# Kernel optimization log

Measured on AMD Instinct MI355X. Metric: run time of the kernel, lower is better.

Reference implementation:

```python
import jax, jax.numpy as jnp
import numpy as np

EMBED_DIM = 1024
NUM_HEADS = 16
HEAD_DIM = EMBED_DIM // NUM_HEADS
SCALE = HEAD_DIM ** -0.5


def setup_inputs() -> dict:
    key = jax.random.key(0)
    ks = jax.random.split(key, 5)
    B, N, C = 4, 2048, EMBED_DIM
    s = C ** -0.5
    return {
        "x": jax.random.normal(ks[0], (B, N, C), dtype=jnp.float32),
        "w_qkv": jax.random.normal(ks[1], (C, 3 * C), dtype=jnp.float32) * s,
        "b_qkv": jnp.zeros((3 * C,), dtype=jnp.float32),
        "w_proj": jax.random.normal(ks[2], (C, C), dtype=jnp.float32) * s,
        "b_proj": jnp.zeros((C,), dtype=jnp.float32),
    }


def reference(x, w_qkv, b_qkv, w_proj, b_proj):
    B, N, C = x.shape
    H, D = NUM_HEADS, HEAD_DIM
    qkv = x @ w_qkv + b_qkv                      # (B, N, 3C)
    qkv = qkv.reshape(B, N, 3, H, D)
    qkv = jnp.transpose(qkv, (2, 0, 3, 1, 4))    # (3, B, H, N, D)
    q, k, v = qkv[0], qkv[1], qkv[2]
    attn = jnp.einsum('bhnd,bhmd->bhnm', q, k) * SCALE
    attn = jax.nn.softmax(attn, axis=-1)
    out = jnp.einsum('bhnm,bhmd->bhnd', attn, v)  # (B, H, N, D)
    out = jnp.transpose(out, (0, 2, 1, 3)).reshape(B, N, C)
    return out @ w_proj + b_proj
```

## Files before the change

### kernel.cpp

```cpp
#include <hip/hip_runtime.h>

typedef __attribute__((ext_vector_type(8))) short short8v;
typedef __attribute__((ext_vector_type(4))) short short4v;
typedef __attribute__((ext_vector_type(4))) float float4v;
typedef __attribute__((ext_vector_type(4))) unsigned short ushort4v;
typedef __attribute__((ext_vector_type(8))) unsigned short ushort8v;

#define GLOBAL_AS __attribute__((address_space(1)))
#define LDS_AS __attribute__((address_space(3)))

__device__ __forceinline__ void async_cp16(const void* g, void* l) {
  __builtin_amdgcn_global_load_lds((const GLOBAL_AS void*)g, (LDS_AS void*)l, 16, 0, 0);
}

__device__ __forceinline__ unsigned short f2bf(float f) {
  unsigned u = __float_as_uint(f);
  u += 0x7fffu + ((u >> 16) & 1u);
  return (unsigned short)(u >> 16);
}

#if defined(__HIP_DEVICE_COMPILE__)
#if __has_builtin(__builtin_amdgcn_exp2f)
#define EXP2F(x) __builtin_amdgcn_exp2f(x)
#else
#define EXP2F(x) exp2f(x)
#endif
#else
#define EXP2F(x) exp2f(x)
#endif

#if defined(__HIP_DEVICE_COMPILE__) && __has_builtin(__builtin_amdgcn_cvt_pk_bf16_f32)
typedef __attribute__((ext_vector_type(2))) __bf16 bf16x2v;
__device__ __forceinline__ unsigned pk_bf16(float a, float b) {
  bf16x2v r = __builtin_amdgcn_cvt_pk_bf16_f32(a, b);
  return __builtin_bit_cast(unsigned, r);
}
#else
__device__ __forceinline__ unsigned pk_bf16(float a, float b) {
  return (unsigned)f2bf(a) | ((unsigned)f2bf(b) << 16);
}
#endif

#define MFMA_QK(a, b, c) __builtin_amdgcn_mfma_f32_16x16x32_bf16(a, b, c, 0, 0, 0)


__global__ __launch_bounds__(256) void cvt_f32_bf16(const float* __restrict__ src,
                                                    unsigned short* __restrict__ dst) {
  int i = blockIdx.x * 256 + threadIdx.x;
  float4 v = ((const float4*)src)[i];
  ushort4v o;
  o.x = f2bf(v.x); o.y = f2bf(v.y); o.z = f2bf(v.z); o.w = f2bf(v.w);
  ((ushort4v*)dst)[i] = o;
}

__global__ __launch_bounds__(256) void transpose_w(const float* __restrict__ src,
                                                   unsigned short* __restrict__ dst,
                                                   int K, int N) {
  __shared__ float tile[64][65];
  int k0 = blockIdx.x * 64, n0 = blockIdx.y * 64;
  int t = threadIdx.x;
  int tc = t & 15, tr = t >> 4;
#pragma unroll
  for (int p = 0; p < 4; p++) {
    int r = tr + p * 16;
    float4 v = *(const float4*)(src + (size_t)(k0 + r) * N + n0 + tc * 4);
    tile[r][tc * 4 + 0] = v.x; tile[r][tc * 4 + 1] = v.y;
    tile[r][tc * 4 + 2] = v.z; tile[r][tc * 4 + 3] = v.w;
  }
  __syncthreads();
#pragma unroll
  for (int p = 0; p < 4; p++) {
    int rn = tr + p * 16;
    ushort4v o;
    o.x = f2bf(tile[tc * 4 + 0][rn]);
    o.y = f2bf(tile[tc * 4 + 1][rn]);
    o.z = f2bf(tile[tc * 4 + 2][rn]);
    o.w = f2bf(tile[tc * 4 + 3][rn]);
    *(ushort4v*)(dst + (size_t)(n0 + rn) * K + k0 + tc * 4) = o;
  }
}

__device__ __forceinline__ void stage128x32(const unsigned short* __restrict__ src,
                                            unsigned short* dst, int r0, int k0, int tid) {
#pragma unroll
  for (int p = 0; p < 2; p++) {
    int idx = p * 256 + tid;
    int row = idx >> 2, s = idx & 3;
    int ch = s ^ ((row >> 1) & 3);
    async_cp16(src + (size_t)(r0 + row) * 1024 + k0 + ch * 8, dst + idx * 8);
  }
}


#define TT_STRIDE 136

__global__ __launch_bounds__(256) void gemm_qkv(const unsigned short* __restrict__ A,
                                                const unsigned short* __restrict__ BT,
                                                const float* __restrict__ bias,
                                                unsigned short* __restrict__ Qo,
                                                unsigned short* __restrict__ Ko,
                                                unsigned short* __restrict__ VTo) {
  __shared__ unsigned short smem[128 * TT_STRIDE];
  unsigned short* As = smem;
  unsigned short* Bs = smem + 4096;
  int tid = threadIdx.x;
  int lane = tid & 63, w = tid >> 6, g = lane >> 4, c = lane & 15;
  int m0 = blockIdx.x * 128, n0 = blockIdx.y * 128;
  int wm = (w & 1) * 64, wn = (w >> 1) * 64;
  float4v acc[4][4] = {};

  for (int k0 = 0; k0 < 1024; k0 += 32) {
    __syncthreads();
    stage128x32(A, As, m0, k0, tid);
    stage128x32(BT, Bs, n0, k0, tid);
    __syncthreads();
    short8v af[4], bf[4];
#pragma unroll
    for (int i = 0; i < 4; i++) {
      int r = wm + i * 16 + c;
      af[i] = *(const short8v*)(&As[r * 32 + (g ^ ((r >> 1) & 3)) * 8]);
    }
#pragma unroll
    for (int j = 0; j < 4; j++) {
      int r = wn + j * 16 + c;
      bf[j] = *(const short8v*)(&Bs[r * 32 + (g ^ ((r >> 1) & 3)) * 8]);
    }
#pragma unroll
    for (int i = 0; i < 4; i++)
#pragma unroll
      for (int j = 0; j < 4; j++)
        acc[i][j] = MFMA_QK(af[i], bf[j], acc[i][j]);
  }

  int which = n0 >> 10;
  if (which != 2) {
#pragma unroll
    for (int j = 0; j < 4; j++) {
      int ng = n0 + wn + j * 16 + c;
      float bv = bias[ng];
      int h = (ng & 1023) >> 6, d = ng & 63;
#pragma unroll
      for (int i = 0; i < 4; i++) {
#pragma unroll
        for (int r = 0; r < 4; r++) {
          int mg = m0 + wm + i * 16 + g * 4 + r;
          int b = mg >> 11, n = mg & 2047;
          float v = acc[i][j][r] + bv;
          if (which == 0)
            Qo[((size_t)(b * 16 + h) * 2048 + n) * 64 + d] = f2bf(v * 0.18033688011112042f);
          else
            Ko[((size_t)(b * 16 + h) * 2048 + n) * 64 + d] = f2bf(v);
        }
      }
    }
  } else {
    __syncthreads();
#pragma unroll
    for (int j = 0; j < 4; j++) {
      int nl = wn + j * 16 + c;
      float bv = bias[n0 + nl];
#pragma unroll
      for (int i = 0; i < 4; i++) {
        int ml = wm + i * 16 + g * 4;
        unsigned p0 = pk_bf16(acc[i][j][0] + bv, acc[i][j][1] + bv);
        unsigned p1 = pk_bf16(acc[i][j][2] + bv, acc[i][j][3] + bv);
        *(unsigned*)(smem + nl * TT_STRIDE + ml) = p0;
        *(unsigned*)(smem + nl * TT_STRIDE + ml + 2) = p1;
      }
    }
    __syncthreads();
    int rr = lane >> 4, tc = lane & 15;
    int P = tc & 3, g32 = tc >> 2;
    int b = m0 >> 11, mloc = m0 & 2047;
    int h0 = (n0 & 1023) >> 6;
#pragma unroll
    for (int s = 0; s < 8; s++) {
      int row = w * 32 + s * 4 + rr;
      int h = h0 + (row >> 6), d = row & 63;
      const unsigned short* bp = smem + row * TT_STRIDE + g32 * 32 + P * 4;
      union { unsigned long long q[2]; ushort8v v; } u;
      u.q[0] = *(const unsigned long long*)(bp);
      u.q[1] = *(const unsigned long long*)(bp + 16);
      size_t gaddr = ((size_t)(b * 16 + h) * 64 + d) * 2048 + mloc + g32 * 32 + P * 8;
      *(ushort8v*)(VTo + gaddr) = u.v;
    }
  }
}


#define NTOK 2048
#define BK 64

__device__ __forceinline__ short8v exppack(float4v a, float4v b2) {
  a.x = EXP2F(a.x); a.y = EXP2F(a.y); a.z = EXP2F(a.z); a.w = EXP2F(a.w);
  b2.x = EXP2F(b2.x); b2.y = EXP2F(b2.y); b2.z = EXP2F(b2.z); b2.w = EXP2F(b2.w);
  union { unsigned u[4]; short8v s; } cv;
  cv.u[0] = pk_bf16(a.x, a.y);
  cv.u[1] = pk_bf16(a.z, a.w);
  cv.u[2] = pk_bf16(b2.x, b2.y);
  cv.u[3] = pk_bf16(b2.z, b2.w);
  return cv.s;
}

__global__ __launch_bounds__(256, 2) void attn_kernel(const unsigned short* __restrict__ Qg,
                                                      const unsigned short* __restrict__ Kg,
                                                      const unsigned short* __restrict__ VTg,
                                                      unsigned short* __restrict__ Og) {
  __shared__ unsigned short Ks[2][BK * 64];
  __shared__ unsigned short VTs[2][64 * BK];

  int tid = threadIdx.x;
  int lane = tid & 63, w = tid >> 6, g = lane >> 4, c = lane & 15;
  int id = blockIdx.x;
  int xcd = id & 7, within = id >> 3;
  int bh = xcd * 8 + (within >> 3);
  int q0 = (within & 7) * 256;

  const unsigned short* Qb = Qg + (size_t)bh * NTOK * 64;
  const unsigned short* Kb = Kg + (size_t)bh * NTOK * 64;
  const unsigned short* VTb = VTg + (size_t)bh * 64 * NTOK;

  short8v qf[4][2];
#pragma unroll
  for (int nt = 0; nt < 4; nt++)
#pragma unroll
    for (int kk = 0; kk < 2; kk++)
      qf[nt][kk] = *(const short8v*)(Qb + (size_t)(q0 + w * 64 + nt * 16 + c) * 64 +
                                     kk * 32 + g * 8);

  short8v ones8;
#pragma unroll
  for (int i = 0; i < 8; i++) ones8[i] = (short)0x3F80;

  float4v lacc[4] = {};
  float4v o[4][4] = {};

#pragma unroll
  for (int p = 0; p < 2; p++) {
    int idx = p * 256 + tid;
    int row = idx >> 3, ch = idx & 7;
    async_cp16(Kb + (size_t)row * 64 + ((ch ^ (row & 7)) * 8), &Ks[0][idx * 8]);
    async_cp16(VTb + (size_t)row * NTOK + ((ch ^ (row & 7)) * 8), &VTs[0][idx * 8]);
  }

  for (int it = 0; it < NTOK / BK; it++) {
    int pb = it & 1;
    __syncthreads();

    if (it + 1 < NTOK / BK) {
      int kt = (it + 1) * BK;
#pragma unroll
      for (int p = 0; p < 2; p++) {
        int idx = p * 256 + tid;
        int row = idx >> 3, ch = idx & 7;
        async_cp16(Kb + (size_t)(kt + row) * 64 + ((ch ^ (row & 7)) * 8),
                   &Ks[1 - pb][idx * 8]);
        async_cp16(VTb + (size_t)row * NTOK + kt + ((ch ^ (row & 7)) * 8),
                   &VTs[1 - pb][idx * 8]);
      }
    }

    const unsigned short* Kp = &Ks[pb][0];
    const unsigned short* Vp = &VTs[pb][0];

    float4v stA[2][4] = {};
    float4v stB[2][4] = {};

    __builtin_amdgcn_s_setprio(1);
#pragma unroll
    for (int mth = 0; mth < 2; mth++) {
      int row = mth * 16 + c;
      short8v kf[2];
#pragma unroll
      for (int kk = 0; kk < 2; kk++) {
        int ch = (kk * 4 + g) ^ (row & 7);
        kf[kk] = *(const short8v*)(Kp + row * 64 + ch * 8);
      }
#pragma unroll
      for (int nt = 0; nt < 4; nt++)
#pragma unroll
        for (int kk = 0; kk < 2; kk++)
          stA[mth][nt] = MFMA_QK(kf[kk], qf[nt][kk], stA[mth][nt]);
    }
#pragma unroll
    for (int mth = 0; mth < 2; mth++) {
      int row = (2 + mth) * 16 + c;
      short8v kf[2];
#pragma unroll
      for (int kk = 0; kk < 2; kk++) {
        int ch = (kk * 4 + g) ^ (row & 7);
        kf[kk] = *(const short8v*)(Kp + row * 64 + ch * 8);
      }
#pragma unroll
      for (int nt = 0; nt < 4; nt++)
#pragma unroll
        for (int kk = 0; kk < 2; kk++)
          stB[mth][nt] = MFMA_QK(kf[kk], qf[nt][kk], stB[mth][nt]);
    }
    __builtin_amdgcn_s_setprio(0);

    short8v pa8A[4];
#pragma unroll
    for (int nt = 0; nt < 4; nt++) pa8A[nt] = exppack(stA[0][nt], stA[1][nt]);

    __builtin_amdgcn_s_setprio(1);
#pragma unroll
    for (int nt_o = 0; nt_o < 4; nt_o++) {
      int d = nt_o * 16 + c;
      int s = g ^ (d & 7);
      short8v vb8 = *(const short8v*)(Vp + d * BK + s * 8);
#pragma unroll
      for (int mt = 0; mt < 4; mt++)
        o[mt][nt_o] = MFMA_QK(pa8A[mt], vb8, o[mt][nt_o]);
    }
#pragma unroll
    for (int mt = 0; mt < 4; mt++)
      lacc[mt] = MFMA_QK(pa8A[mt], ones8, lacc[mt]);
    __builtin_amdgcn_s_setprio(0);

    short8v pa8B[4];
#pragma unroll
    for (int nt = 0; nt < 4; nt++) pa8B[nt] = exppack(stB[0][nt], stB[1][nt]);

    __builtin_amdgcn_s_setprio(1);
#pragma unroll
    for (int nt_o = 0; nt_o < 4; nt_o++) {
      int d = nt_o * 16 + c;
      int s = (4 + g) ^ (d & 7);
      short8v vb8 = *(const short8v*)(Vp + d * BK + s * 8);
#pragma unroll
      for (int mt = 0; mt < 4; mt++)
        o[mt][nt_o] = MFMA_QK(pa8B[mt], vb8, o[mt][nt_o]);
    }
#pragma unroll
    for (int mt = 0; mt < 4; mt++)
      lacc[mt] = MFMA_QK(pa8B[mt], ones8, lacc[mt]);
    __builtin_amdgcn_s_setprio(0);
  }

  int b = bh >> 4, h = bh & 15;
#pragma unroll
  for (int mt = 0; mt < 4; mt++) {
    float4v li;
#pragma unroll
    for (int r = 0; r < 4; r++) li[r] = 1.0f / lacc[mt][r];
#pragma unroll
    for (int nt_o = 0; nt_o < 4; nt_o++) {
      float4v v = o[mt][nt_o] * li;
      int col = h * 64 + nt_o * 16 + c;
      int rowbase = b * NTOK + q0 + w * 64 + mt * 16 + g * 4;
#pragma unroll
      for (int r = 0; r < 4; r++)
        Og[(size_t)(rowbase + r) * 1024 + col] = f2bf(v[r]);
    }
  }
}

__global__ __launch_bounds__(256) void gemm_proj(const unsigned short* __restrict__ A,
                                                 const unsigned short* __restrict__ BT,
                                                 const float* __restrict__ bias,
                                                 float* __restrict__ out) {
  __shared__ unsigned short As[128 * 32];
  __shared__ unsigned short Bs[128 * 32];
  int tid = threadIdx.x;
  int lane = tid & 63, w = tid >> 6, g = lane >> 4, c = lane & 15;
  int m0 = blockIdx.x * 128, n0 = blockIdx.y * 128;
  int wm = (w & 1) * 64, wn = (w >> 1) * 64;
  float4v acc[4][4] = {};

  for (int k0 = 0; k0 < 1024; k0 += 32) {
    __syncthreads();
    stage128x32(A, As, m0, k0, tid);
    stage128x32(BT, Bs, n0, k0, tid);
    __syncthreads();
    short8v af[4], bf[4];
#pragma unroll
    for (int i = 0; i < 4; i++) {
      int r = wm + i * 16 + c;
      af[i] = *(const short8v*)(&As[r * 32 + (g ^ ((r >> 1) & 3)) * 8]);
    }
#pragma unroll
    for (int j = 0; j < 4; j++) {
      int r = wn + j * 16 + c;
      bf[j] = *(const short8v*)(&Bs[r * 32 + (g ^ ((r >> 1) & 3)) * 8]);
    }
#pragma unroll
    for (int i = 0; i < 4; i++)
#pragma unroll
      for (int j = 0; j < 4; j++)
        acc[i][j] = MFMA_QK(af[i], bf[j], acc[i][j]);
  }

#pragma unroll
  for (int j = 0; j < 4; j++) {
    int ng = n0 + wn + j * 16 + c;
    float bv = bias[ng];
#pragma unroll
    for (int i = 0; i < 4; i++) {
#pragma unroll
      for (int r = 0; r < 4; r++) {
        int mg = m0 + wm + i * 16 + g * 4 + r;
        out[(size_t)mg * 1024 + ng] = acc[i][j][r] + bv;
      }
    }
  }
}


extern "C" void kernel_launch(void* const* d_in, const int* in_sizes, int n_in,
                              void* d_out, int out_size, void* d_ws, size_t ws_size,
                              hipStream_t stream) {
  (void)in_sizes; (void)n_in; (void)out_size; (void)ws_size;
  const float* x = (const float*)d_in[0];
  const float* w_qkv = (const float*)d_in[1];
  const float* b_qkv = (const float*)d_in[2];
  const float* w_proj = (const float*)d_in[3];
  const float* b_proj = (const float*)d_in[4];
  float* out = (float*)d_out;

  unsigned short* x_bf = (unsigned short*)d_ws;
  unsigned short* wqkvT = x_bf + (size_t)8192 * 1024;
  unsigned short* wprojT = wqkvT + (size_t)3072 * 1024;
  unsigned short* qws = wprojT + (size_t)1024 * 1024;
  unsigned short* kws = qws + (size_t)8388608;
  unsigned short* vtws = kws + (size_t)8388608;
  unsigned short* aws = vtws + (size_t)8388608;

  cvt_f32_bf16<<<8192, 256, 0, stream>>>(x, x_bf);
  transpose_w<<<dim3(16, 48), 256, 0, stream>>>(w_qkv, wqkvT, 1024, 3072);
  transpose_w<<<dim3(16, 16), 256, 0, stream>>>(w_proj, wprojT, 1024, 1024);
  gemm_qkv<<<dim3(64, 24), 256, 0, stream>>>(x_bf, wqkvT, b_qkv, qws, kws, vtws);
  attn_kernel<<<512, 256, 0, stream>>>(qws, kws, vtws, aws);
  gemm_proj<<<dim3(64, 8), 256, 0, stream>>>(aws, wprojT, b_proj, out);
}
```

Baseline: 274.6 us.

## Triple-buffer async LDS staging in QKV and projection GEMMs

Replaces the load-sync-compute loop in both GEMM kernels with a three-stage ring of LDS buffers, prefetching tiles two K-steps ahead via async global-to-LDS copies. It uses partial vmcnt waits and a single barrier per iteration so memory latency overlaps MFMA work, and raises wave priority during the MFMA block. LDS usage grows, which may reduce occupancy.

```diff
diff --git a/kernel.cpp b/kernel.cpp
--- a/kernel.cpp
+++ b/kernel.cpp
@@ -43,6 +43,12 @@
 
 #define MFMA_QK(a, b, c) __builtin_amdgcn_mfma_f32_16x16x32_bf16(a, b, c, 0, 0, 0)
 
+__device__ __forceinline__ void wg_barrier() {
+  asm volatile("" ::: "memory");
+  __builtin_amdgcn_s_barrier();
+  asm volatile("" ::: "memory");
+}
+
 
 __global__ __launch_bounds__(256) void cvt_f32_bf16(const float* __restrict__ src,
                                                     unsigned short* __restrict__ dst) {
@@ -100,36 +106,55 @@
                                                 unsigned short* __restrict__ Qo,
                                                 unsigned short* __restrict__ Ko,
                                                 unsigned short* __restrict__ VTo) {
-  __shared__ unsigned short smem[128 * TT_STRIDE];
-  unsigned short* As = smem;
-  unsigned short* Bs = smem + 4096;
+  __shared__ unsigned short smem[24576];
   int tid = threadIdx.x;
   int lane = tid & 63, w = tid >> 6, g = lane >> 4, c = lane & 15;
   int m0 = blockIdx.x * 128, n0 = blockIdx.y * 128;
   int wm = (w & 1) * 64, wn = (w >> 1) * 64;
   float4v acc[4][4] = {};
 
-  for (int k0 = 0; k0 < 1024; k0 += 32) {
-    __syncthreads();
-    stage128x32(A, As, m0, k0, tid);
-    stage128x32(BT, Bs, n0, k0, tid);
-    __syncthreads();
+  stage128x32(A, smem + 0 * 4096, m0, 0, tid);
+  stage128x32(BT, smem + 12288 + 0 * 4096, n0, 0, tid);
+  stage128x32(A, smem + 1 * 4096, m0, 32, tid);
+  stage128x32(BT, smem + 12288 + 1 * 4096, n0, 32, tid);
+  asm volatile("s_waitcnt vmcnt(4)" ::: "memory");
+  wg_barrier();
+
+  int cb = 0;
+  for (int t = 0; t < 32; ++t) {
+    int nb = cb + 2; if (nb >= 3) nb -= 3;
+    const unsigned short* Ap = smem + cb * 4096;
+    const unsigned short* Bp = smem + 12288 + cb * 4096;
+
     short8v af[4], bf[4];
 #pragma unroll
     for (int i = 0; i < 4; i++) {
       int r = wm + i * 16 + c;
-      af[i] = *(const short8v*)(&As[r * 32 + (g ^ ((r >> 1) & 3)) * 8]);
+      af[i] = *(const short8v*)(Ap + r * 32 + (g ^ ((r >> 1) & 3)) * 8);
     }
 #pragma unroll
     for (int j = 0; j < 4; j++) {
       int r = wn + j * 16 + c;
-      bf[j] = *(const short8v*)(&Bs[r * 32 + (g ^ ((r >> 1) & 3)) * 8]);
-    }
+      bf[j] = *(const short8v*)(Bp + r * 32 + (g ^ ((r >> 1) & 3)) * 8);
+    }
+
+    if (t + 2 < 32) {
+      stage128x32(A, smem + nb * 4096, m0, (t + 2) * 32, tid);
+      stage128x32(BT, smem + 12288 + nb * 4096, n0, (t + 2) * 32, tid);
+    }
+
+    __builtin_amdgcn_s_setprio(1);
 #pragma unroll
     for (int i = 0; i < 4; i++)
 #pragma unroll
       for (int j = 0; j < 4; j++)
         acc[i][j] = MFMA_QK(af[i], bf[j], acc[i][j]);
+    __builtin_amdgcn_s_setprio(0);
+
+    if (t < 30) { asm volatile("s_waitcnt vmcnt(4)" ::: "memory"); }
+    else        { asm volatile("s_waitcnt vmcnt(0)" ::: "memory"); }
+    wg_barrier();
+    cb = cb + 1 == 3 ? 0 : cb + 1;
   }
 
   int which = n0 >> 10;
@@ -360,35 +385,55 @@
                                                  const unsigned short* __restrict__ BT,
                                                  const float* __restrict__ bias,
                                                  float* __restrict__ out) {
-  __shared__ unsigned short As[128 * 32];
-  __shared__ unsigned short Bs[128 * 32];
+  __shared__ unsigned short smem[24576];
   int tid = threadIdx.x;
   int lane = tid & 63, w = tid >> 6, g = lane >> 4, c = lane & 15;
   int m0 = blockIdx.x * 128, n0 = blockIdx.y * 128;
   int wm = (w & 1) * 64, wn = (w >> 1) * 64;
   float4v acc[4][4] = {};
 
-  for (int k0 = 0; k0 < 1024; k0 += 32) {
-    __syncthreads();
-    stage128x32(A, As, m0, k0, tid);
-    stage128x32(BT, Bs, n0, k0, tid);
-    __syncthreads();
+  stage128x32(A, smem + 0 * 4096, m0, 0, tid);
+  stage128x32(BT, smem + 12288 + 0 * 4096, n0, 0, tid);
+  stage128x32(A, smem + 1 * 4096, m0, 32, tid);
+  stage128x32(BT, smem + 12288 + 1 * 4096, n0, 32, tid);
+  asm volatile("s_waitcnt vmcnt(4)" ::: "memory");
+  wg_barrier();
+
+  int cb = 0;
+  for (int t = 0; t < 32; ++t) {
+    int nb = cb + 2; if (nb >= 3) nb -= 3;
+    const unsigned short* Ap = smem + cb * 4096;
+    const unsigned short* Bp = smem + 12288 + cb * 4096;
+
     short8v af[4], bf[4];
 #pragma unroll
     for (int i = 0; i < 4; i++) {
       int r = wm + i * 16 + c;
-      af[i] = *(const short8v*)(&As[r * 32 + (g ^ ((r >> 1) & 3)) * 8]);
+      af[i] = *(const short8v*)(Ap + r * 32 + (g ^ ((r >> 1) & 3)) * 8);
     }
 #pragma unroll
     for (int j = 0; j < 4; j++) {
       int r = wn + j * 16 + c;
-      bf[j] = *(const short8v*)(&Bs[r * 32 + (g ^ ((r >> 1) & 3)) * 8]);
-    }
+      bf[j] = *(const short8v*)(Bp + r * 32 + (g ^ ((r >> 1) & 3)) * 8);
+    }
+
+    if (t + 2 < 32) {
+      stage128x32(A, smem + nb * 4096, m0, (t + 2) * 32, tid);
+      stage128x32(BT, smem + 12288 + nb * 4096, n0, (t + 2) * 32, tid);
+    }
+
+    __builtin_amdgcn_s_setprio(1);
 #pragma unroll
     for (int i = 0; i < 4; i++)
 #pragma unroll
       for (int j = 0; j < 4; j++)
         acc[i][j] = MFMA_QK(af[i], bf[j], acc[i][j]);
+    __builtin_amdgcn_s_setprio(0);
+
+    if (t < 30) { asm volatile("s_waitcnt vmcnt(4)" ::: "memory"); }
+    else        { asm volatile("s_waitcnt vmcnt(0)" ::: "memory"); }
+    wg_barrier();
+    cb = cb + 1 == 3 ? 0 : cb + 1;
   }
 
 #pragma unroll
```

Measured after the change: 265.9 us. 1.03x faster.
